# Performance work log

Measured on AMD Instinct MI355X. Metric: run time of the kernel, lower is better.

The kernel has to match this reference:

```python
import jax, jax.numpy as jnp
import numpy as np

B, M, N = 32, 256, 4000          # images, gt boxes/img, proposals/img
NUM_CLASSES = 80                 # cfg.MODEL.ROI_HEADS.NUM_CLASSES
BATCH_PER_IMG = 512              # cfg.MODEL.ROI_HEADS.BATCH_SIZE_PER_IMAGE
POS_FRAC = 0.25                  # cfg.MODEL.ROI_HEADS.POSITIVE_FRACTION
IOU_THRESH = 0.5                 # cfg.MODEL.ROI_HEADS.IOU_THRESHOLDS
IMG_SIZE = 1024.0


def _make_boxes(key, shape):
    # valid xyxy boxes: centers in [0, IMG_SIZE], sides in [4, 256]
    k1, k2 = jax.random.split(key)
    c = jax.random.uniform(k1, shape[:-1] + (2,)) * IMG_SIZE
    wh = 4.0 + jax.random.uniform(k2, shape[:-1] + (2,)) * 252.0
    return jnp.concatenate([c - wh / 2, c + wh / 2], axis=-1)


def setup_inputs() -> dict:
    key = jax.random.key(0)
    kg, kp, kc, kr = jax.random.split(key, 4)
    gt_boxes = _make_boxes(kg, (B, M, 4))
    proposal_boxes = _make_boxes(kp, (B, N, 4))
    gt_classes = jax.random.randint(kc, (B, M), 0, NUM_CLASSES, dtype=jnp.int32)
    # random priorities stand in for torch.randperm in subsample_labels
    rand_priority = jax.random.uniform(kr, (B, N + M))
    return {"gt_boxes": gt_boxes, "proposal_boxes": proposal_boxes,
            "gt_classes": gt_classes, "rand_priority": rand_priority}


def _pairwise_iou(b1, b2):
    # b1 [M,4], b2 [K,4] -> [M,K]  (detectron2 pairwise_iou)
    a1 = (b1[:, 2] - b1[:, 0]) * (b1[:, 3] - b1[:, 1])
    a2 = (b2[:, 2] - b2[:, 0]) * (b2[:, 3] - b2[:, 1])
    lt = jnp.maximum(b1[:, None, :2], b2[None, :, :2])
    rb = jnp.minimum(b1[:, None, 2:], b2[None, :, 2:])
    wh = jnp.clip(rb - lt, 0.0)
    inter = wh[..., 0] * wh[..., 1]
    union = a1[:, None] + a2[None, :] - inter
    return jnp.where(inter > 0, inter / union, 0.0)


def _rank_desc(score):
    # rank of each element in descending order of score
    order = jnp.argsort(-score)
    return jnp.zeros_like(order).at[order].set(jnp.arange(order.shape[0]))


def _per_image(gt_b, prop_b, gt_c, pri):
    # add_ground_truth_to_proposals (proposal_append_gt=True)
    boxes = jnp.concatenate([prop_b, gt_b], axis=0)          # [N+M, 4]
    iou = _pairwise_iou(gt_b, boxes)                          # [M, N+M]
    # Matcher(thresholds=[0.5], labels=[0,1], allow_low_quality=False)
    matched_idxs = jnp.argmax(iou, axis=0)                    # [N+M]
    matched_vals = jnp.max(iou, axis=0)
    matched_labels = (matched_vals >= IOU_THRESH).astype(jnp.int32)
    # _sample_proposals: assign classes, bg where label==0
    cls = gt_c[matched_idxs]
    cls = jnp.where(matched_labels == 0, NUM_CLASSES, cls)
    # subsample_labels with random priorities (fixed-shape, jit-safe)
    fg = cls < NUM_CLASSES
    bg = cls == NUM_CLASSES
    num_fg = jnp.minimum(fg.sum(), int(BATCH_PER_IMG * POS_FRAC))
    num_bg = jnp.minimum(bg.sum(), BATCH_PER_IMG - num_fg)
    sel_fg = fg & (_rank_desc(jnp.where(fg, pri, -jnp.inf)) < num_fg)
    sel_bg = bg & (_rank_desc(jnp.where(bg, pri, -jnp.inf)) < num_bg)
    sel = sel_fg | sel_bg
    _, idx = jax.lax.top_k(jnp.where(sel, pri, -jnp.inf), BATCH_PER_IMG)
    labels = jnp.where(sel[idx], cls[idx], -1)                # pad -1 if <512 valid
    return iou, matched_idxs, matched_labels, idx, labels


def reference(gt_boxes, proposal_boxes, gt_classes, rand_priority):
    return jax.vmap(_per_image)(gt_boxes, proposal_boxes, gt_classes, rand_priority)
```

## Files before the change

### kernel.cpp

```cpp
#include <hip/hip_runtime.h>
#include <hip/hip_bf16.h>

#define Bimg 32
#define Mgt 256
#define Nprop 4000
#define KBOX (Nprop + Mgt)
#define NCLS 80
#define BATCH 512
#define NFG_CAP 128
#define NBINS 1024
#define BINCAP 1024
#define MT 32
#define MS (Mgt / MT)
#define CPT 2
#define KCH ((KBOX + 256*CPT - 1) / (256*CPT))

typedef float f32x2 __attribute__((ext_vector_type(2)));
typedef unsigned long long ull;

__global__ __launch_bounds__(256) void iou_part_kernel(
    const float* __restrict__ gt_boxes,
    const float* __restrict__ prop_boxes,
    float* __restrict__ out_iou,
    ull* __restrict__ part)
{
    const int b  = blockIdx.z;
    const int ms = blockIdx.y;
    const int m0 = ms * MT;
    const int k0 = (blockIdx.x * 256 + threadIdx.x) * CPT;

    __shared__ float4 gbox[MT];
    __shared__ float  garea[MT];
    if (threadIdx.x < MT) {
        float4 g = ((const float4*)(gt_boxes + (size_t)b * Mgt * 4))[m0 + threadIdx.x];
        gbox[threadIdx.x] = g;
        garea[threadIdx.x] = (g.z - g.x) * (g.w - g.y);
    }
    __syncthreads();
    if (k0 >= KBOX) return;

    float4 bx[CPT]; float a2[CPT];
    if (k0 < Nprop) {
        const float4* pp = (const float4*)(prop_boxes + (size_t)b * Nprop * 4);
        #pragma unroll
        for (int c = 0; c < CPT; ++c) bx[c] = pp[k0 + c];
    } else {
        const float4* gg = (const float4*)(gt_boxes + (size_t)b * Mgt * 4);
        #pragma unroll
        for (int c = 0; c < CPT; ++c) bx[c] = gg[k0 - Nprop + c];
    }
    #pragma unroll
    for (int c = 0; c < CPT; ++c) a2[c] = (bx[c].z - bx[c].x) * (bx[c].w - bx[c].y);

    float bestv[CPT]; int bestm[CPT];
    #pragma unroll
    for (int c = 0; c < CPT; ++c) { bestv[c] = -1.f; bestm[c] = 0; }
    float* orow = out_iou + (size_t)b * Mgt * KBOX + (size_t)m0 * KBOX + k0;

    for (int mm = 0; mm < MT; ++mm) {
        float4 g = gbox[mm];
        float ga = garea[mm];
        float io[CPT];
        #pragma unroll
        for (int c = 0; c < CPT; ++c) {
            float ltx = fmaxf(g.x, bx[c].x), lty = fmaxf(g.y, bx[c].y);
            float rbx = fminf(g.z, bx[c].z), rby = fminf(g.w, bx[c].w);
            float w = fmaxf(rbx - ltx, 0.0f);
            float h = fmaxf(rby - lty, 0.0f);
            float inter = w * h;
            float uni = ga + a2[c] - inter;
            float iou = (inter > 0.0f) ? (inter / uni) : 0.0f;
            io[c] = iou;
            if (iou > bestv[c]) { bestv[c] = iou; bestm[c] = m0 + mm; }
        }
        f32x2 res = { io[0], io[1] };
        *(f32x2*)(orow + (size_t)mm * KBOX) = res;
    }

    ull* pr = part + ((size_t)b * MS + ms) * KBOX + k0;
    ull bk0 = ((ull)__float_as_uint(bestv[0]) << 8) | (ull)(255 - bestm[0]);
    ull bk1 = ((ull)__float_as_uint(bestv[1]) << 8) | (ull)(255 - bestm[1]);
    *(ulonglong2*)pr = make_ulonglong2(bk0, bk1);
}

__global__ __launch_bounds__(1024) void sample_kernel(
    const int*   __restrict__ gt_classes,
    const float* __restrict__ pri,
    const ull*   __restrict__ part,
    float* __restrict__ out_midx,
    float* __restrict__ out_mlab,
    float* __restrict__ out_idx,
    float* __restrict__ out_lab)
{
    const int b    = blockIdx.x;
    const int tid  = threadIdx.x;
    const int lane = tid & 63;
    const int wv   = tid >> 6;

    __shared__ ull keys[KBOX];
    __shared__ unsigned char selA[KBOX];
    __shared__ int gcls[Mgt];
    __shared__ int histP[NBINS];
    __shared__ int sufP[NBINS + 1];
    __shared__ ull binFG[BINCAP];
    __shared__ ull binBG[BINCAP];
    __shared__ __align__(16) ull selKeys[BATCH + 2];
    __shared__ int waveTot[16], waveOff[16];
    __shared__ int cntF, cntB, cntSel, sTF, sTB;

    histP[tid] = 0;
    if (tid < Mgt) gcls[tid] = gt_classes[b * Mgt + tid];
    if (tid == 0) { cntF = 0; cntB = 0; cntSel = 0; sTF = -1; sTB = -1; }
    __syncthreads();

    for (int i = tid; i < KBOX; i += 1024) {
        float p  = pri[(size_t)b * KBOX + i];
        ull bk = part[(size_t)b * MS * KBOX + i];
        #pragma unroll
        for (int s = 1; s < MS; ++s) {
            ull k2 = part[((size_t)b * MS + s) * KBOX + i];
            if (k2 > bk) bk = k2;
        }
        float v  = __uint_as_float((unsigned)(bk >> 8));
        int   mi = 255 - (int)(bk & 0xFFull);
        bool  fg = (v >= 0.5f);
        int  cls = fg ? gcls[mi] : NCLS;
        out_midx[(size_t)b * KBOX + i] = (float)mi;
        out_mlab[(size_t)b * KBOX + i] = fg ? 1.0f : 0.0f;
        unsigned pb = __float_as_uint(p);
        keys[i] = ((ull)pb << 32) |
                  ((ull)(0xFFFFu - (unsigned)i) << 16) |
                  ((ull)(unsigned)cls << 8);
        selA[i] = 0;
        int bucket = (int)(p * (float)NBINS);
        bucket = min(max(bucket, 0), NBINS - 1);
        atomicAdd(&histP[bucket], fg ? 1 : (1 << 16));
    }
    __syncthreads();

    int v = histP[tid];
    #pragma unroll
    for (int off = 1; off < 64; off <<= 1) {
        int o = __shfl_down(v, off);
        if (lane + off < 64) v += o;
    }
    if (lane == 0) waveTot[wv] = v;
    __syncthreads();
    if (wv == 0) {
        int t = (lane < 16) ? waveTot[lane] : 0;
        #pragma unroll
        for (int off = 1; off < 64; off <<= 1) {
            int o = __shfl_down(t, off);
            if (lane + off < 64) t += o;
        }
        if (lane < 16) waveOff[lane] = t - waveTot[lane];
    }
    __syncthreads();
    sufP[tid] = v + waveOff[wv];
    if (tid == 0) sufP[NBINS] = 0;
    __syncthreads();

    const int total_fg = sufP[0] & 0xFFFF;
    const int total_bg = (sufP[0] >> 16) & 0xFFFF;
    const int num_fg = min(total_fg, NFG_CAP);
    const int num_bg = min(total_bg, BATCH - num_fg);

    {
        int sf  = sufP[tid] & 0xFFFF;
        int sfn = sufP[tid + 1] & 0xFFFF;
        if (num_fg > 0 && sf >= num_fg && sfn < num_fg) sTF = tid;
        int sb  = (sufP[tid] >> 16) & 0xFFFF;
        int sbn = (sufP[tid + 1] >> 16) & 0xFFFF;
        if (num_bg > 0 && sb >= num_bg && sbn < num_bg) sTB = tid;
    }
    __syncthreads();
    const int tF = sTF, tB = sTB;
    const int aboveF = (tF >= 0) ? (sufP[tF + 1] & 0xFFFF) : 0;
    const int aboveB = (tB >= 0) ? ((sufP[tB + 1] >> 16) & 0xFFFF) : 0;
    const int needF = num_fg - aboveF;
    const int needB = num_bg - aboveB;

    for (int i = tid; i < KBOX; i += 1024) {
        ull key = keys[i];
        float p = __uint_as_float((unsigned)(key >> 32));
        int bucket = (int)(p * (float)NBINS);
        bucket = min(max(bucket, 0), NBINS - 1);
        bool fg = ((unsigned)(key >> 8) & 0xFFu) < NCLS;
        if (fg) {
            if (tF >= 0) {
                if (bucket > tF) selA[i] = 1;
                else if (bucket == tF) { int j = atomicAdd(&cntF, 1); if (j < BINCAP) binFG[j] = key; }
            }
        } else {
            if (tB >= 0) {
                if (bucket > tB) selA[i] = 1;
                else if (bucket == tB) { int j = atomicAdd(&cntB, 1); if (j < BINCAP) binBG[j] = key; }
            }
        }
    }
    __syncthreads();

    {
        int cf = min(cntF, BINCAP);
        for (int j = tid; j < cf; j += 1024) {
            ull key = binFG[j];
            int rank = 0;
            for (int l = 0; l < cf; ++l) rank += (binFG[l] > key) ? 1 : 0;
            if (rank < needF) { unsigned kk = 0xFFFFu - (unsigned)((key >> 16) & 0xFFFFu); selA[kk] = 1; }
        }
        int cb = min(cntB, BINCAP);
        for (int j = tid; j < cb; j += 1024) {
            ull key = binBG[j];
            int rank = 0;
            for (int l = 0; l < cb; ++l) rank += (binBG[l] > key) ? 1 : 0;
            if (rank < needB) { unsigned kk = 0xFFFFu - (unsigned)((key >> 16) & 0xFFFFu); selA[kk] = 1; }
        }
    }
    __syncthreads();

    for (int i = tid; i < KBOX; i += 1024) {
        if (selA[i]) {
            int p = atomicAdd(&cntSel, 1);
            selKeys[p] = keys[i];
        }
    }
    __syncthreads();
    const int ns = cntSel;
    if (tid == 0) { selKeys[ns] = 0ull; selKeys[ns + 1] = 0ull; }
    __syncthreads();

    if (tid < ns) {
        ull key = selKeys[tid];
        int rank = 0;
        const int n2 = (ns + 1) & ~1;
        for (int l = 0; l < n2; l += 2) {
            ulonglong2 two = *(const ulonglong2*)&selKeys[l];
            rank += (two.x > key) ? 1 : 0;
            rank += (two.y > key) ? 1 : 0;
        }
        unsigned kk = 0xFFFFu - (unsigned)((key >> 16) & 0xFFFFu);
        int cls = (int)((key >> 8) & 0xFFu);
        out_idx[b * BATCH + rank] = (float)kk;
        out_lab[b * BATCH + rank] = (float)cls;
    }

    if (ns < BATCH) {
        __syncthreads();
        int loc[5]; int acc = 0;
        #pragma unroll
        for (int q = 0; q < 5; ++q) {
            int i = tid * 5 + q;
            int contrib = (i < KBOX && !selA[i]) ? 1 : 0;
            loc[q] = acc; acc += contrib;
        }
        histP[tid] = acc;
        __syncthreads();
        for (int off = 1; off < 1024; off <<= 1) {
            int vv = histP[tid];
            int add = (tid >= off) ? histP[tid - off] : 0;
            __syncthreads();
            histP[tid] = vv + add;
            __syncthreads();
        }
        int excl = tid ? histP[tid - 1] : 0;
        #pragma unroll
        for (int q = 0; q < 5; ++q) {
            int i = tid * 5 + q;
            if (i < KBOX && !selA[i]) {
                int p = ns + excl + loc[q];
                if (p < BATCH) { out_idx[b * BATCH + p] = (float)i; out_lab[b * BATCH + p] = -1.0f; }
            }
        }
    }
}

extern "C" void kernel_launch(void* const* d_in, const int* in_sizes, int n_in,
                              void* d_out, int out_size, void* d_ws, size_t ws_size,
                              hipStream_t stream) {
    const float* gt_boxes   = (const float*)d_in[0];
    const float* prop_boxes = (const float*)d_in[1];
    const int*   gt_classes = (const int*)d_in[2];
    const float* rand_pri   = (const float*)d_in[3];

    float* out = (float*)d_out;
    const size_t off_iou  = 0;
    const size_t off_midx = (size_t)Bimg * Mgt * KBOX;
    const size_t off_mlab = off_midx + (size_t)Bimg * KBOX;
    const size_t off_idx  = off_mlab + (size_t)Bimg * KBOX;
    const size_t off_lab  = off_idx  + (size_t)Bimg * BATCH;

    ull* part = (ull*)d_ws;

    dim3 gridA(KCH, MS, Bimg);
    iou_part_kernel<<<gridA, 256, 0, stream>>>(
        gt_boxes, prop_boxes, out + off_iou, part);

    sample_kernel<<<Bimg, 1024, 0, stream>>>(
        gt_classes, rand_pri, part,
        out + off_midx, out + off_mlab,
        out + off_idx, out + off_lab);
}
```

Baseline: 60.04 us.

## Split per-image decode into a wide parallel kernel and use fast reciprocal IoU

The partial-argmax reduction, class lookup, key building and histogram work moves out of the 32-block sample kernel into a new decode kernel. That kernel runs over many blocks per image and writes keys and per-chunk histograms to workspace, which the sample kernel then loads and sums. The IoU division is replaced by a hardware reciprocal followed by one Newton refinement step. The cost is an extra launch and a workspace round trip, and the IoU values may differ slightly in the last bits.

```diff
diff --git a/kernel.cpp b/kernel.cpp
--- a/kernel.cpp
+++ b/kernel.cpp
@@ -14,6 +14,7 @@
 #define MS (Mgt / MT)
 #define CPT 2
 #define KCH ((KBOX + 256*CPT - 1) / (256*CPT))
+#define KCHB ((KBOX + 511) / 512)
 
 typedef float f32x2 __attribute__((ext_vector_type(2)));
 typedef unsigned long long ull;
@@ -69,7 +70,10 @@
             float h = fmaxf(rby - lty, 0.0f);
             float inter = w * h;
             float uni = ga + a2[c] - inter;
-            float iou = (inter > 0.0f) ? (inter / uni) : 0.0f;
+            float r = __builtin_amdgcn_rcpf(uni);
+            r = fmaf(fmaf(-uni, r, 1.0f), r, r);
+            float iou = inter * r;
+            iou = (inter > 0.0f) ? iou : 0.0f;
             io[c] = iou;
             if (iou > bestv[c]) { bestv[c] = iou; bestm[c] = m0 + mm; }
         }
@@ -83,12 +87,67 @@
     *(ulonglong2*)pr = make_ulonglong2(bk0, bk1);
 }
 
-__global__ __launch_bounds__(1024) void sample_kernel(
+__global__ __launch_bounds__(256) void decode_kernel(
     const int*   __restrict__ gt_classes,
     const float* __restrict__ pri,
     const ull*   __restrict__ part,
     float* __restrict__ out_midx,
     float* __restrict__ out_mlab,
+    ull*   __restrict__ keysG,
+    int*   __restrict__ histG)
+{
+    const int b   = blockIdx.y;
+    const int ch  = blockIdx.x;
+    const int tid = threadIdx.x;
+
+    __shared__ int histL[NBINS];
+    __shared__ int gcls[Mgt];
+    *(int4*)&histL[tid * 4] = make_int4(0, 0, 0, 0);
+    gcls[tid] = gt_classes[b * Mgt + tid];
+    __syncthreads();
+
+    const int i0 = ch * 512 + tid * 2;
+    if (i0 < KBOX) {
+        const ull* p0 = part + (size_t)b * MS * KBOX + i0;
+        ulonglong2 bk2 = *(const ulonglong2*)p0;
+        ull bk[2] = { bk2.x, bk2.y };
+        #pragma unroll
+        for (int s = 1; s < MS; ++s) {
+            ulonglong2 t = *(const ulonglong2*)(p0 + (size_t)s * KBOX);
+            bk[0] = (t.x > bk[0]) ? t.x : bk[0];
+            bk[1] = (t.y > bk[1]) ? t.y : bk[1];
+        }
+        f32x2 pv = *(const f32x2*)(pri + (size_t)b * KBOX + i0);
+        float mi2[2], ml2[2]; ull kk[2];
+        #pragma unroll
+        for (int c = 0; c < 2; ++c) {
+            float v  = __uint_as_float((unsigned)(bk[c] >> 8));
+            int   mi = 255 - (int)(bk[c] & 0xFFull);
+            bool  fg = (v >= 0.5f);
+            int  cls = fg ? gcls[mi] : NCLS;
+            mi2[c] = (float)mi;
+            ml2[c] = fg ? 1.0f : 0.0f;
+            float p = pv[c];
+            unsigned pb = __float_as_uint(p);
+            kk[c] = ((ull)pb << 32) |
+                    ((ull)(0xFFFFu - (unsigned)(i0 + c)) << 16) |
+                    ((ull)(unsigned)cls << 8);
+            int bucket = (int)(p * (float)NBINS);
+            bucket = min(max(bucket, 0), NBINS - 1);
+            atomicAdd(&histL[bucket], fg ? 1 : (1 << 16));
+        }
+        *(f32x2*)(out_midx + (size_t)b * KBOX + i0) = f32x2{ mi2[0], mi2[1] };
+        *(f32x2*)(out_mlab + (size_t)b * KBOX + i0) = f32x2{ ml2[0], ml2[1] };
+        *(ulonglong2*)(keysG + (size_t)b * KBOX + i0) = make_ulonglong2(kk[0], kk[1]);
+    }
+    __syncthreads();
+    int4 h = *(int4*)&histL[tid * 4];
+    *(int4*)&histG[((size_t)(b * KCHB + ch)) * NBINS + tid * 4] = h;
+}
+
+__global__ __launch_bounds__(1024) void sample_kernel(
+    const ull* __restrict__ keysG,
+    const int* __restrict__ histG,
     float* __restrict__ out_idx,
     float* __restrict__ out_lab)
 {
@@ -99,46 +158,27 @@
 
     __shared__ ull keys[KBOX];
     __shared__ unsigned char selA[KBOX];
-    __shared__ int gcls[Mgt];
-    __shared__ int histP[NBINS];
     __shared__ int sufP[NBINS + 1];
+    __shared__ int scanT[NBINS];
     __shared__ ull binFG[BINCAP];
     __shared__ ull binBG[BINCAP];
     __shared__ __align__(16) ull selKeys[BATCH + 2];
     __shared__ int waveTot[16], waveOff[16];
     __shared__ int cntF, cntB, cntSel, sTF, sTB;
 
-    histP[tid] = 0;
-    if (tid < Mgt) gcls[tid] = gt_classes[b * Mgt + tid];
+    for (int i0 = tid * 4; i0 < KBOX; i0 += 1024 * 4) {
+        ulonglong2 a = *(const ulonglong2*)(keysG + (size_t)b * KBOX + i0);
+        ulonglong2 c = *(const ulonglong2*)(keysG + (size_t)b * KBOX + i0 + 2);
+        *(ulonglong2*)&keys[i0]     = a;
+        *(ulonglong2*)&keys[i0 + 2] = c;
+        *(uchar4*)&selA[i0] = make_uchar4(0, 0, 0, 0);
+    }
+    int hv = 0;
+    #pragma unroll
+    for (int c = 0; c < KCHB; ++c) hv += histG[((size_t)(b * KCHB + c)) * NBINS + tid];
     if (tid == 0) { cntF = 0; cntB = 0; cntSel = 0; sTF = -1; sTB = -1; }
-    __syncthreads();
-
-    for (int i = tid; i < KBOX; i += 1024) {
-        float p  = pri[(size_t)b * KBOX + i];
-        ull bk = part[(size_t)b * MS * KBOX + i];
-        #pragma unroll
-        for (int s = 1; s < MS; ++s) {
-            ull k2 = part[((size_t)b * MS + s) * KBOX + i];
-            if (k2 > bk) bk = k2;
-        }
-        float v  = __uint_as_float((unsigned)(bk >> 8));
-        int   mi = 255 - (int)(bk & 0xFFull);
-        bool  fg = (v >= 0.5f);
-        int  cls = fg ? gcls[mi] : NCLS;
-        out_midx[(size_t)b * KBOX + i] = (float)mi;
-        out_mlab[(size_t)b * KBOX + i] = fg ? 1.0f : 0.0f;
-        unsigned pb = __float_as_uint(p);
-        keys[i] = ((ull)pb << 32) |
-                  ((ull)(0xFFFFu - (unsigned)i) << 16) |
-                  ((ull)(unsigned)cls << 8);
-        selA[i] = 0;
-        int bucket = (int)(p * (float)NBINS);
-        bucket = min(max(bucket, 0), NBINS - 1);
-        atomicAdd(&histP[bucket], fg ? 1 : (1 << 16));
-    }
-    __syncthreads();
-
-    int v = histP[tid];
+
+    int v = hv;
     #pragma unroll
     for (int off = 1; off < 64; off <<= 1) {
         int o = __shfl_down(v, off);
@@ -253,16 +293,16 @@
             int contrib = (i < KBOX && !selA[i]) ? 1 : 0;
             loc[q] = acc; acc += contrib;
         }
-        histP[tid] = acc;
+        scanT[tid] = acc;
         __syncthreads();
         for (int off = 1; off < 1024; off <<= 1) {
-            int vv = histP[tid];
-            int add = (tid >= off) ? histP[tid - off] : 0;
+            int vv = scanT[tid];
+            int add = (tid >= off) ? scanT[tid - off] : 0;
             __syncthreads();
-            histP[tid] = vv + add;
+            scanT[tid] = vv + add;
             __syncthreads();
         }
-        int excl = tid ? histP[tid - 1] : 0;
+        int excl = tid ? scanT[tid - 1] : 0;
         #pragma unroll
         for (int q = 0; q < 5; ++q) {
             int i = tid * 5 + q;
@@ -289,14 +329,21 @@
     const size_t off_idx  = off_mlab + (size_t)Bimg * KBOX;
     const size_t off_lab  = off_idx  + (size_t)Bimg * BATCH;
 
-    ull* part = (ull*)d_ws;
+    char* ws = (char*)d_ws;
+    ull* part  = (ull*)ws;
+    ull* keysG = (ull*)(ws + (size_t)Bimg * MS * KBOX * 8);
+    int* histG = (int*)(ws + (size_t)Bimg * MS * KBOX * 8
+                           + (size_t)Bimg * KBOX * 8);
 
     dim3 gridA(KCH, MS, Bimg);
     iou_part_kernel<<<gridA, 256, 0, stream>>>(
         gt_boxes, prop_boxes, out + off_iou, part);
 
+    dim3 gridD(KCHB, Bimg);
+    decode_kernel<<<gridD, 256, 0, stream>>>(
+        gt_classes, rand_pri, part,
+        out + off_midx, out + off_mlab, keysG, histG);
+
     sample_kernel<<<Bimg, 1024, 0, stream>>>(
-        gt_classes, rand_pri, part,
-        out + off_midx, out + off_mlab,
-        out + off_idx, out + off_lab);
+        keysG, histG, out + off_idx, out + off_lab);
 }
```

After: 57.66 us. -4.0%, faster.
